# Kernel optimization log

Measured on AMD Instinct MI355X. Metric: run time of the kernel, lower is better.

The kernel has to match this reference:

```python
import jax, jax.numpy as jnp
import numpy as np

T, N, F = 32, 100000, 2
E = 1600000
H4 = 4 * F  # PyTorch LSTM packs gates i,f,g,o


def setup_inputs() -> dict:
    key = jax.random.key(0)
    ks = jax.random.split(key, 8)
    stdv = 1.0 / np.sqrt(F)
    x = jax.random.normal(ks[0], (T, N, F), dtype=jnp.float32)
    edge_index = jax.random.randint(ks[1], (2, E), 0, N, dtype=jnp.int32)
    mask = jax.random.randint(ks[2], (N,), 0, 2, dtype=jnp.int32).astype(bool)
    labels = jnp.zeros((N,), dtype=jnp.int32)
    edge_weight = jnp.ones((E,), dtype=jnp.float32)
    data = 0  # unused placeholder (pyg Data object in original)
    w_ih = jax.random.uniform(ks[3], (H4, F), minval=-stdv, maxval=stdv, dtype=jnp.float32)
    w_hh = jax.random.uniform(ks[4], (H4, F), minval=-stdv, maxval=stdv, dtype=jnp.float32)
    b_ih = jax.random.uniform(ks[5], (H4,), minval=-stdv, maxval=stdv, dtype=jnp.float32)
    b_hh = jax.random.uniform(ks[6], (H4,), minval=-stdv, maxval=stdv, dtype=jnp.float32)
    return {"x": x, "edge_index": edge_index, "mask": mask, "labels": labels,
            "edge_weight": edge_weight, "data": data,
            "w_ih": w_ih, "w_hh": w_hh, "b_ih": b_ih, "b_hh": b_hh}


def _interpolate(x, src, dst, n_nodes):
    # Iteratively fill zero entries with the mean over neighbors whose node
    # has any nonzero data (matches A[row_no_data,:]=0 edge filtering).
    def cond(carry):
        xx, i = carry
        return jnp.logical_and(jnp.any(xx == 0), i < 20)

    def body(carry):
        xx, i = carry
        has_data = jnp.sum(xx != 0, axis=(0, 2)) > 0            # [N]
        valid = has_data[src].astype(xx.dtype)                   # [E]
        msg = xx[:, src, :] * valid[None, :, None]               # [T,E,F]
        agg = jax.ops.segment_sum(jnp.transpose(msg, (1, 0, 2)), dst,
                                  num_segments=n_nodes)          # [N,T,F]
        cnt = jax.ops.segment_sum(valid, dst, num_segments=n_nodes)  # [N]
        mean = jnp.transpose(agg, (1, 0, 2)) / jnp.where(cnt > 0, cnt, 1.0)[None, :, None]
        return jnp.where(xx == 0, mean, xx), i + 1

    out, _ = jax.lax.while_loop(cond, body, (x, jnp.int32(0)))
    return out


def _lstm(x_seq, w_ih, w_hh, b_ih, b_hh):
    # x_seq: [T, N, F]; single-layer LSTM, hidden size F, gate order i,f,g,o.
    n, h = x_seq.shape[1], w_hh.shape[1]
    def step(carry, xt):
        hp, cp = carry
        g = xt @ w_ih.T + b_ih + hp @ w_hh.T + b_hh              # [N, 4F]
        i_, f_, g_, o_ = jnp.split(g, 4, axis=-1)
        i_ = jax.nn.sigmoid(i_); f_ = jax.nn.sigmoid(f_)
        g_ = jnp.tanh(g_);        o_ = jax.nn.sigmoid(o_)
        c = f_ * cp + i_ * g_
        hh = o_ * jnp.tanh(c)
        return (hh, c), hh
    z = jnp.zeros((n, h), dtype=x_seq.dtype)
    _, out = jax.lax.scan(step, (z, z), x_seq)
    return out


def reference(x, edge_index, mask, labels, edge_weight, data, w_ih, w_hh, b_ih, b_hh):
    masked = jnp.where(mask[None, :, None], x, jnp.zeros((), x.dtype))
    src, dst = edge_index[0], edge_index[1]
    interp_x = _interpolate(masked, src, dst, x.shape[1])
    return _lstm(interp_x, w_ih, w_hh, b_ih, b_hh)
```

## Files before the change

kernel.cpp:

```cpp
#include <hip/hip_runtime.h>
#include <math.h>

#define TT    32
#define NN    100000
#define FF    2
#define ROW   64
#define EE    1600000
#define MAXIT 20
#define LDSROW 66
#define BIGIT (1 << 29)
#define NR    8
#define RNG   (NN / NR)
#define SLOT  28
#define QCAP   131072
#define IQCAP  442368
#define CIDCAP 2048
#define CHUNK  782

typedef float f32x4 __attribute__((ext_vector_type(4)));
typedef float f32x2 __attribute__((ext_vector_type(2)));

__device__ __forceinline__ float fsig(float x) { return 1.0f / (1.0f + __expf(-x)); }
__device__ __forceinline__ float ftanh(float x) { return 2.0f / (1.0f + __expf(-2.0f * x)) - 1.0f; }

__global__ void k_mt_flags(const float* __restrict__ x, const int* __restrict__ mask,
                           float* __restrict__ xx, int* __restrict__ fill_iter,
                           unsigned char* __restrict__ hz, unsigned char* __restrict__ hd,
                           int* __restrict__ cnt_v, int* __restrict__ cidmap,
                           int* __restrict__ icnt, int* __restrict__ qc,
                           int* __restrict__ wl_count) {
    __shared__ float tile[64 * LDSROW];
    const int n0 = blockIdx.x * 64;
    const int tid = threadIdx.x;

    if (tid < 64 && n0 + tid < NN) { cnt_v[n0 + tid] = 0; cidmap[n0 + tid] = 0; }
    if (blockIdx.x == 0) {
        if (tid < 32) wl_count[tid] = 0;
        if (tid >= 64 && tid < 80) qc[tid - 64] = 0;
    }
    if (blockIdx.x < 8) icnt[blockIdx.x * 256 + tid] = 0;

#pragma unroll
    for (int r = 0; r < 16; r++) {
        int flat = r * 256 + tid;
        int t = flat >> 7;
        int col = flat & 127;
        int gcol = n0 * 2 + col;
        if (gcol < NN * FF) {
            int n = n0 + (col >> 1);
            float v = __builtin_nontemporal_load(x + (size_t)t * (NN * FF) + gcol);
            v = mask[n] ? v : 0.0f;
            tile[(col >> 1) * LDSROW + t * 2 + (col & 1)] = v;
        }
    }
    __syncthreads();

    const int lane = tid & 63, w = tid >> 6;
    for (int i = 0; i < 16; i++) {
        int ln = w * 16 + i;
        int n = n0 + ln;
        if (n >= NN) break;
        float v = tile[ln * LDSROW + lane];
        unsigned long long nzm = __ballot(v != 0.0f);
        if (lane == 0) {
            fill_iter[n] = (nzm != 0ull) ? 0 : BIGIT;
            hz[n] = (nzm != ~0ull) ? 1 : 0;
            hd[n] = (nzm != 0ull) ? 1 : 0;
        }
    }

#pragma unroll
    for (int j = 0; j < 4; j++) {
        int flat4 = j * 256 + tid;
        int ln = flat4 >> 4;
        int n = n0 + ln;
        if (n >= NN) continue;
        int off = (flat4 & 15) * 4;
        float4 v;
        v.x = tile[ln * LDSROW + off + 0];
        v.y = tile[ln * LDSROW + off + 1];
        v.z = tile[ln * LDSROW + off + 2];
        v.w = tile[ln * LDSROW + off + 3];
        *(float4*)(xx + (size_t)n * ROW + off) = v;
    }
}

__global__ void k_compact(const int* __restrict__ ei, const unsigned char* __restrict__ hz,
                          const unsigned char* __restrict__ hd,
                          int2* __restrict__ vq, int2* __restrict__ iq,
                          int* __restrict__ qc) {
    __shared__ int lcnt[9];
    __shared__ int lbase[9];
    const int tid = threadIdx.x;
    if (tid < 9) lcnt[tid] = 0;
    __syncthreads();
    const int e0 = blockIdx.x * CHUNK;
    const int e1 = min(e0 + CHUNK, EE);
    int rs[4], rd[4], rb[4], rp[4];
#pragma unroll
    for (int i = 0; i < 4; i++) {
        rb[i] = -1;
        int e = e0 + i * 256 + tid;
        if (e < e1) {
            int dst = __builtin_nontemporal_load(ei + EE + e);
            if (hz[dst]) {
                int src = __builtin_nontemporal_load(ei + e);
                int b = hd[src] ? (dst / RNG) : 8;
                rs[i] = src; rd[i] = dst; rb[i] = b;
                rp[i] = atomicAdd(&lcnt[b], 1);
            }
        }
    }
    __syncthreads();
    if (tid < 9) lbase[tid] = atomicAdd(&qc[tid], lcnt[tid]);
    __syncthreads();
#pragma unroll
    for (int i = 0; i < 4; i++) {
        if (rb[i] >= 0) {
            int b = rb[i];
            int p = lbase[b] + rp[i];
            if (b < 8) { if (p < QCAP)  vq[b * QCAP + p] = make_int2(rs[i], rd[i]); }
            else       { if (p < IQCAP) iq[p]            = make_int2(rs[i], rd[i]); }
        }
    }
}

__global__ void k_build(const int2* __restrict__ vq, const int* __restrict__ qc,
                        int* __restrict__ cnt_v, int* __restrict__ slab) {
    const int r = blockIdx.x & 7;
    int n = qc[r]; if (n > QCAP) n = QCAP;
    const int gid = (blockIdx.x >> 3) * blockDim.x + threadIdx.x;
    const int stride = (gridDim.x >> 3) * blockDim.x;
    const int2* q = vq + r * QCAP;
    for (int i = gid; i < n; i += stride) {
        int2 sd = q[i];
        int pos = atomicAdd(&cnt_v[sd.y], 1);
        if (pos < SLOT) slab[sd.y * SLOT + pos] = sd.x;
    }
}

__global__ void k_inv(const int2* __restrict__ iq, const int* __restrict__ qc,
                      const int* __restrict__ cnt_v, int* __restrict__ cidmap,
                      int* __restrict__ icnt, int* __restrict__ islab,
                      int* __restrict__ ncid) {
    int n = qc[8]; if (n > IQCAP) n = IQCAP;
    const int gid = blockIdx.x * blockDim.x + threadIdx.x;
    const int stride = gridDim.x * blockDim.x;
    for (int i = gid; i < n; i += stride) {
        int2 sd = iq[i];
        if (cnt_v[sd.y] != 0) continue;
        int cid = cidmap[sd.y];
        if (cid == 0) {
            int nid = atomicAdd(ncid, 1) + 1;
            int old = atomicCAS(&cidmap[sd.y], 0, nid);
            cid = old ? old : nid;
        }
        if (cid <= CIDCAP) {
            int pos = atomicAdd(&icnt[cid - 1], 1);
            if (pos < SLOT) islab[(cid - 1) * SLOT + pos] = sd.x;
        }
    }
}

__device__ __forceinline__ void gather_node4(int n, int k, int lane,
                                             int vbeg, int vend, const int* __restrict__ vsl,
                                             int ibeg, int iend, const int* __restrict__ isl,
                                             int* __restrict__ fill_iter,
                                             float* __restrict__ xx,
                                             int* __restrict__ wl_next,
                                             int* __restrict__ wl_count) {
    const int g = lane >> 4;
    const int s = lane & 15;
    float ax = 0.f, ay = 0.f, az = 0.f, aw = 0.f, cntv = 0.f;
#pragma unroll 2
    for (int e = vbeg + g; e < vend; e += 4) {
        int src = vsl[e];
        f32x4 v = ((const f32x4*)(xx + (size_t)src * ROW))[s];
        ax += v.x; ay += v.y; az += v.z; aw += v.w; cntv += 1.f;
    }
    for (int e = ibeg + g; e < iend; e += 4) {
        int src = isl[e];
        if (fill_iter[src] < k) {
            f32x4 v = ((const f32x4*)(xx + (size_t)src * ROW))[s];
            ax += v.x; ay += v.y; az += v.z; aw += v.w; cntv += 1.f;
        }
    }
#pragma unroll
    for (int d = 16; d <= 32; d <<= 1) {
        ax += __shfl_xor(ax, d, 64);
        ay += __shfl_xor(ay, d, 64);
        az += __shfl_xor(az, d, 64);
        aw += __shfl_xor(aw, d, 64);
        cntv += __shfl_xor(cntv, d, 64);
    }
    f32x4 own = ((const f32x4*)(xx + (size_t)n * ROW))[s];
    bool has = cntv > 0.f;
    f32x4 nv;
    nv.x = (own.x == 0.f && has) ? ax / cntv : own.x;
    nv.y = (own.y == 0.f && has) ? ay / cntv : own.y;
    nv.z = (own.z == 0.f && has) ? az / cntv : own.z;
    nv.w = (own.w == 0.f && has) ? aw / cntv : own.w;
    bool allnz = (nv.x != 0.f) & (nv.y != 0.f) & (nv.z != 0.f) & (nv.w != 0.f);
    bool anynz = (nv.x != 0.f) | (nv.y != 0.f) | (nv.z != 0.f) | (nv.w != 0.f);
    unsigned long long ba = __ballot(allnz);
    unsigned long long bn = __ballot(anynz);
    if (g == 0) ((f32x4*)(xx + (size_t)n * ROW))[s] = nv;
    if (lane == 0) {
        if (bn != 0ull && fill_iter[n] > k) fill_iter[n] = k;
        if (ba != ~0ull) {
            int pos = atomicAdd(&wl_count[k], 1);
            wl_next[pos] = n;
        }
    }
}

__global__ void k_gather_first(const unsigned char* __restrict__ hz,
                               const int* __restrict__ cnt_v, const int* __restrict__ slab,
                               int* __restrict__ fill_iter, float* __restrict__ xx,
                               int* __restrict__ wl_next, int* __restrict__ wl_count) {
    const int lane = threadIdx.x & 63;
    int wave = (blockIdx.x * blockDim.x + threadIdx.x) >> 6;
    const int nwaves = (gridDim.x * blockDim.x) >> 6;
    for (int n0 = wave; n0 < NN; n0 += nwaves) {
        int n = __builtin_amdgcn_readfirstlane(n0);
        if (!hz[n]) continue;
        int cv = cnt_v[n]; if (cv > SLOT) cv = SLOT;
        gather_node4(n, 1, lane, n * SLOT, n * SLOT + cv, slab, 0, 0, slab,
                     fill_iter, xx, wl_next, wl_count);
    }
}

__global__ __launch_bounds__(1024)
void k_gather_rest(int* __restrict__ wl_a, int* __restrict__ wl_b,
                   int* __restrict__ wl_count,
                   const int* __restrict__ cnt_v, const int* __restrict__ cidmap,
                   const int* __restrict__ icnt, const int* __restrict__ islab,
                   const int* __restrict__ slab,
                   int* __restrict__ fill_iter, float* __restrict__ xx) {
    const int lane = threadIdx.x & 63;
    const int wave = threadIdx.x >> 6;
    for (int k = 2; k <= MAXIT; k++) {
        int cnt = atomicAdd(&wl_count[k - 1], 0);
        if (cnt == 0) break;
        int* prev = (k & 1) ? wl_b : wl_a;
        int* next = (k & 1) ? wl_a : wl_b;
        for (int w = wave; w < cnt; w += 16) {
            int n = __builtin_amdgcn_readfirstlane(prev[w]);
            int cv = cnt_v[n]; if (cv > SLOT) cv = SLOT;
            int cid = cidmap[n];
            int ci = 0, ib = 0;
            if (cid > 0 && cid <= CIDCAP) {
                ci = icnt[cid - 1]; if (ci > SLOT) ci = SLOT;
                ib = (cid - 1) * SLOT;
            }
            gather_node4(n, k, lane, n * SLOT, n * SLOT + cv, slab,
                         ib, ib + ci, islab,
                         fill_iter, xx, next, wl_count);
        }
        __threadfence();
        __syncthreads();
    }
}

__global__ void k_lstm(const float* __restrict__ xx,
                       const float* __restrict__ wih, const float* __restrict__ whh,
                       const float* __restrict__ bih, const float* __restrict__ bhh,
                       float* __restrict__ out) {
    int n = blockIdx.x * 64 + threadIdx.x;
    if (n >= NN) return;
    float Wi[8][2], Wh[8][2], B[8];
#pragma unroll
    for (int kk = 0; kk < 8; kk++) {
        Wi[kk][0] = wih[kk * 2]; Wi[kk][1] = wih[kk * 2 + 1];
        Wh[kk][0] = whh[kk * 2]; Wh[kk][1] = whh[kk * 2 + 1];
        B[kk] = bih[kk] + bhh[kk];
    }
    f32x4 r4[16];
    const f32x4* row4 = (const f32x4*)(xx + (size_t)n * ROW);
#pragma unroll
    for (int i = 0; i < 16; i++) r4[i] = __builtin_nontemporal_load(row4 + i);

    float h0 = 0.f, h1 = 0.f, c0 = 0.f, c1 = 0.f;
#pragma unroll
    for (int t = 0; t < TT; t++) {
        f32x4 q = r4[t >> 1];
        float x0 = (t & 1) ? q.z : q.x;
        float x1 = (t & 1) ? q.w : q.y;
        float g[8];
#pragma unroll
        for (int kk = 0; kk < 8; kk++)
            g[kk] = B[kk] + Wi[kk][0] * x0 + Wi[kk][1] * x1 + Wh[kk][0] * h0 + Wh[kk][1] * h1;
        float i0 = fsig(g[0]), i1 = fsig(g[1]);
        float f0 = fsig(g[2]), f1 = fsig(g[3]);
        float gg0 = ftanh(g[4]), gg1 = ftanh(g[5]);
        float o0 = fsig(g[6]), o1 = fsig(g[7]);
        c0 = f0 * c0 + i0 * gg0;
        c1 = f1 * c1 + i1 * gg1;
        h0 = o0 * ftanh(c0);
        h1 = o1 * ftanh(c1);
        f32x2 hv; hv.x = h0; hv.y = h1;
        __builtin_nontemporal_store(hv, (f32x2*)(out + (size_t)t * (NN * FF) + n * 2));
    }
}

extern "C" void kernel_launch(void* const* d_in, const int* in_sizes, int n_in,
                              void* d_out, int out_size, void* d_ws, size_t ws_size,
                              hipStream_t stream) {
    const float* x    = (const float*)d_in[0];
    const int*   ei   = (const int*)d_in[1];
    const int*   mask = (const int*)d_in[2];
    const float* wih  = (const float*)d_in[6];
    const float* whh  = (const float*)d_in[7];
    const float* bih  = (const float*)d_in[8];
    const float* bhh  = (const float*)d_in[9];
    float* out = (float*)d_out;

    char* ws = (char*)d_ws;
    float* xx        = (float*)ws;
    int*   fill_iter = (int*)(ws + (size_t)NN * ROW * 4);
    int*   wl_count  = fill_iter + NN;
    unsigned char* hz = (unsigned char*)(wl_count + 32);
    unsigned char* hd = hz + ((NN + 15) & ~15);

    int*  slab   = (int*)d_out;
    int2* vq     = (int2*)(slab + (size_t)NN * SLOT);
    int2* iq     = vq + 8 * (size_t)QCAP;
    int*  cnt_v  = (int*)(iq + IQCAP);
    int*  cidmap = cnt_v + NN;
    int*  wl_a   = cidmap + NN;
    int*  wl_b   = wl_a + NN;
    int*  icnt   = wl_b + NN;
    int*  islab  = icnt + CIDCAP;
    int*  qc     = islab + CIDCAP * SLOT;

    k_mt_flags<<<(NN + 63) / 64, 256, 0, stream>>>(x, mask, xx, fill_iter, hz, hd,
                                                   cnt_v, cidmap, icnt, qc, wl_count);
    k_compact<<<(EE + CHUNK - 1) / CHUNK, 256, 0, stream>>>(ei, hz, hd, vq, iq, qc);
    k_build<<<2048, 256, 0, stream>>>(vq, qc, cnt_v, slab);
    k_inv<<<512, 256, 0, stream>>>(iq, qc, cnt_v, cidmap, icnt, islab, qc + 9);
    k_gather_first<<<6250, 256, 0, stream>>>(hz, cnt_v, slab, fill_iter, xx, wl_a, wl_count);
    k_gather_rest<<<1, 1024, 0, stream>>>(wl_a, wl_b, wl_count, cnt_v, cidmap, icnt, islab,
                                          slab, fill_iter, xx);
    k_lstm<<<(NN + 63) / 64, 64, 0, stream>>>(xx, wih, whh, bih, bhh, out);
}
```

Before: 246.2 us.

## Build compact worklist of zero-containing nodes and vectorize input transpose loads

The flag kernel now loads the input with 4-wide nontemporal loads and writes float2 pairs into shared memory. Each wave also compacts the indices of nodes with any zero entry into a worklist using an atomic counter. The first gather pass walks only that worklist on a smaller grid instead of scanning every node and checking a flag. It also skips reading a node's own row when the node had no data at all. The counters are now cleared by a memset before launch, which adds one extra API call and an atomic per wave.

After: 298.3 us. +21.1%, slower.

```diff
diff --git a/kernel.cpp b/kernel.cpp
--- a/kernel.cpp
+++ b/kernel.cpp
@@ -28,44 +28,67 @@
                            unsigned char* __restrict__ hz, unsigned char* __restrict__ hd,
                            int* __restrict__ cnt_v, int* __restrict__ cidmap,
                            int* __restrict__ icnt, int* __restrict__ qc,
-                           int* __restrict__ wl_count) {
+                           int* __restrict__ wl_hz, int* __restrict__ wl_count) {
     __shared__ float tile[64 * LDSROW];
     const int n0 = blockIdx.x * 64;
     const int tid = threadIdx.x;
 
     if (tid < 64 && n0 + tid < NN) { cnt_v[n0 + tid] = 0; cidmap[n0 + tid] = 0; }
-    if (blockIdx.x == 0) {
-        if (tid < 32) wl_count[tid] = 0;
-        if (tid >= 64 && tid < 80) qc[tid - 64] = 0;
-    }
+    if (blockIdx.x == 0 && tid < 32) wl_count[tid] = 0;
     if (blockIdx.x < 8) icnt[blockIdx.x * 256 + tid] = 0;
 
 #pragma unroll
-    for (int r = 0; r < 16; r++) {
-        int flat = r * 256 + tid;
+    for (int it = 0; it < 4; it++) {
+        int flat = (it * 256 + tid) * 4;
         int t = flat >> 7;
-        int col = flat & 127;
-        int gcol = n0 * 2 + col;
-        if (gcol < NN * FF) {
-            int n = n0 + (col >> 1);
-            float v = __builtin_nontemporal_load(x + (size_t)t * (NN * FF) + gcol);
-            v = mask[n] ? v : 0.0f;
-            tile[(col >> 1) * LDSROW + t * 2 + (col & 1)] = v;
-        }
+        int c0 = flat & 127;
+        int gbase = n0 * 2 + c0;
+        const float* xp = x + (size_t)t * (NN * FF) + gbase;
+        f32x4 v;
+        if (gbase + 3 < NN * FF) {
+            v = __builtin_nontemporal_load((const f32x4*)xp);
+        } else {
+            v.x = (gbase + 0 < NN * FF) ? xp[0] : 0.0f;
+            v.y = (gbase + 1 < NN * FF) ? xp[1] : 0.0f;
+            v.z = (gbase + 2 < NN * FF) ? xp[2] : 0.0f;
+            v.w = (gbase + 3 < NN * FF) ? xp[3] : 0.0f;
+        }
+        int nA = n0 + (c0 >> 1);
+        int nB = nA + 1;
+        if (!(nA < NN && mask[nA])) { v.x = 0.0f; v.y = 0.0f; }
+        if (!(nB < NN && mask[nB])) { v.z = 0.0f; v.w = 0.0f; }
+        *(float2*)&tile[(c0 >> 1) * LDSROW + t * 2]       = make_float2(v.x, v.y);
+        *(float2*)&tile[((c0 >> 1) + 1) * LDSROW + t * 2] = make_float2(v.z, v.w);
     }
     __syncthreads();
 
     const int lane = tid & 63, w = tid >> 6;
+    unsigned int mwave = 0;
     for (int i = 0; i < 16; i++) {
         int ln = w * 16 + i;
         int n = n0 + ln;
         if (n >= NN) break;
         float v = tile[ln * LDSROW + lane];
         unsigned long long nzm = __ballot(v != 0.0f);
+        bool hzv = (nzm != ~0ull);
+        if (hzv) mwave |= (1u << i);
         if (lane == 0) {
             fill_iter[n] = (nzm != 0ull) ? 0 : BIGIT;
-            hz[n] = (nzm != ~0ull) ? 1 : 0;
+            hz[n] = hzv ? 1 : 0;
             hd[n] = (nzm != 0ull) ? 1 : 0;
+        }
+    }
+
+    {
+        bool sel = (lane < 16) && ((mwave >> lane) & 1u);
+        unsigned long long bal = __ballot(sel);
+        int cnt = __popcll(bal);
+        int b0 = 0;
+        if (lane == 0 && cnt) b0 = atomicAdd(&qc[10], cnt);
+        int base = __builtin_amdgcn_readfirstlane(b0);
+        if (sel) {
+            int pos = base + __popcll(bal & ((1ull << lane) - 1ull));
+            wl_hz[pos] = n0 + w * 16 + lane;
         }
     }
 
@@ -162,7 +185,7 @@
     }
 }
 
-__device__ __forceinline__ void gather_node4(int n, int k, int lane,
+__device__ __forceinline__ void gather_node4(int n, int k, int lane, bool zrow,
                                              int vbeg, int vend, const int* __restrict__ vsl,
                                              int ibeg, int iend, const int* __restrict__ isl,
                                              int* __restrict__ fill_iter,
@@ -193,7 +216,9 @@
         aw += __shfl_xor(aw, d, 64);
         cntv += __shfl_xor(cntv, d, 64);
     }
-    f32x4 own = ((const f32x4*)(xx + (size_t)n * ROW))[s];
+    f32x4 own;
+    if (zrow) { own.x = 0.f; own.y = 0.f; own.z = 0.f; own.w = 0.f; }
+    else        own = ((const f32x4*)(xx + (size_t)n * ROW))[s];
     bool has = cntv > 0.f;
     f32x4 nv;
     nv.x = (own.x == 0.f && has) ? ax / cntv : own.x;
@@ -214,18 +239,19 @@
     }
 }
 
-__global__ void k_gather_first(const unsigned char* __restrict__ hz,
+__global__ void k_gather_first(const int* __restrict__ wl_hz, const int* __restrict__ qc,
                                const int* __restrict__ cnt_v, const int* __restrict__ slab,
                                int* __restrict__ fill_iter, float* __restrict__ xx,
                                int* __restrict__ wl_next, int* __restrict__ wl_count) {
     const int lane = threadIdx.x & 63;
     int wave = (blockIdx.x * blockDim.x + threadIdx.x) >> 6;
     const int nwaves = (gridDim.x * blockDim.x) >> 6;
-    for (int n0 = wave; n0 < NN; n0 += nwaves) {
-        int n = __builtin_amdgcn_readfirstlane(n0);
-        if (!hz[n]) continue;
+    const int cnt = __builtin_amdgcn_readfirstlane(qc[10]);
+    for (int w = wave; w < cnt; w += nwaves) {
+        int n = __builtin_amdgcn_readfirstlane(wl_hz[w]);
         int cv = cnt_v[n]; if (cv > SLOT) cv = SLOT;
-        gather_node4(n, 1, lane, n * SLOT, n * SLOT + cv, slab, 0, 0, slab,
+        bool zrow = (__builtin_amdgcn_readfirstlane(fill_iter[n]) == BIGIT);
+        gather_node4(n, 1, lane, zrow, n * SLOT, n * SLOT + cv, slab, 0, 0, slab,
                      fill_iter, xx, wl_next, wl_count);
     }
 }
@@ -253,7 +279,8 @@
                 ci = icnt[cid - 1]; if (ci > SLOT) ci = SLOT;
                 ib = (cid - 1) * SLOT;
             }
-            gather_node4(n, k, lane, n * SLOT, n * SLOT + cv, slab,
+            bool zrow = (__builtin_amdgcn_readfirstlane(fill_iter[n]) == BIGIT);
+            gather_node4(n, k, lane, zrow, n * SLOT, n * SLOT + cv, slab,
                          ib, ib + ci, islab,
                          fill_iter, xx, next, wl_count);
         }
@@ -332,13 +359,16 @@
     int*  icnt   = wl_b + NN;
     int*  islab  = icnt + CIDCAP;
     int*  qc     = islab + CIDCAP * SLOT;
-
+    int*  wl_hz  = qc + 16;
+
+    (void)hipMemsetAsync(qc, 0, 64, stream);
     k_mt_flags<<<(NN + 63) / 64, 256, 0, stream>>>(x, mask, xx, fill_iter, hz, hd,
-                                                   cnt_v, cidmap, icnt, qc, wl_count);
+                                                   cnt_v, cidmap, icnt, qc, wl_hz, wl_count);
     k_compact<<<(EE + CHUNK - 1) / CHUNK, 256, 0, stream>>>(ei, hz, hd, vq, iq, qc);
     k_build<<<2048, 256, 0, stream>>>(vq, qc, cnt_v, slab);
     k_inv<<<512, 256, 0, stream>>>(iq, qc, cnt_v, cidmap, icnt, islab, qc + 9);
-    k_gather_first<<<6250, 256, 0, stream>>>(hz, cnt_v, slab, fill_iter, xx, wl_a, wl_count);
+    k_gather_first<<<2048, 256, 0, stream>>>(wl_hz, qc, cnt_v, slab, fill_iter, xx,
+                                             wl_a, wl_count);
     k_gather_rest<<<1, 1024, 0, stream>>>(wl_a, wl_b, wl_count, cnt_v, cidmap, icnt, islab,
                                           slab, fill_iter, xx);
     k_lstm<<<(NN + 63) / 64, 64, 0, stream>>>(xx, wih, whh, bih, bhh, out);
```
